# Kernel optimization log

Measured on AMD Instinct MI355X. Metric: run time of the kernel, lower is better.

## Reference

```python
import jax, jax.numpy as jnp
import numpy as np

B, N, D = 8, 2048, 1024

def setup_inputs() -> dict:
    key = jax.random.key(0)
    ks = jax.random.split(key, 7)
    s = 1.0 / np.sqrt(D)
    return {
        "x": jax.random.normal(ks[0], (B, N, D), dtype=jnp.float32),
        "Wq": jax.random.uniform(ks[1], (D, D), jnp.float32, -s, s),
        "bq": jax.random.uniform(ks[2], (D,), jnp.float32, -s, s),
        "Wk": jax.random.uniform(ks[3], (D, D), jnp.float32, -s, s),
        "bk": jax.random.uniform(ks[4], (D,), jnp.float32, -s, s),
        "Wv": jax.random.uniform(ks[5], (D, D), jnp.float32, -s, s),
        "bv": jax.random.uniform(ks[6], (D,), jnp.float32, -s, s),
    }

def reference(x, Wq, bq, Wk, bk, Wv, bv):
    # torch nn.Linear: y = x @ W.T + b
    q = jnp.einsum('bnd,ed->bne', x, Wq) + bq
    k = jnp.einsum('bnd,ed->bne', x, Wk) + bk
    v = jnp.einsum('bnd,ed->bne', x, Wv) + bv
    # NOTE: original applies NO 1/sqrt(d) scaling
    scores = jnp.einsum('bnd,bmd->bnm', q, k)  # [B, N, N]
    probs = jax.nn.softmax(scores, axis=-1)
    return jnp.einsum('bnm,bmd->bnd', probs, v)
```

## Files before the change

### kernel.cpp

```cpp
#include <hip/hip_runtime.h>


typedef _Float16 f16;
typedef _Float16 f16x4 __attribute__((ext_vector_type(4)));
typedef _Float16 f16x8 __attribute__((ext_vector_type(8)));
typedef float f32x4 __attribute__((ext_vector_type(4)));

#define Nn_ 2048
#define Dd 1024

typedef const __attribute__((address_space(1))) void gvoid;
typedef __attribute__((address_space(3))) void lvoid;

__device__ __forceinline__ void glds16(const void* g, void* l) {
    __builtin_amdgcn_global_load_lds((gvoid*)g, (lvoid*)l, 16, 0, 0);
}
__device__ __forceinline__ void bar_vm3() {
    asm volatile("s_waitcnt vmcnt(3)\n\ts_barrier" ::: "memory");
}
__device__ __forceinline__ void bar_vm0() {
    asm volatile("s_waitcnt vmcnt(0)\n\ts_barrier" ::: "memory");
}

__global__ void cvt_kernel(const float4* __restrict__ in, f16x4* __restrict__ out, int n4) {
    int i = blockIdx.x * 256 + threadIdx.x;
    if (i >= n4) return;
    float4 f = in[i];
    f16x4 h;
    h.x = (_Float16)f.x; h.y = (_Float16)f.y; h.z = (_Float16)f.z; h.w = (_Float16)f.w;
    out[i] = h;
}

__global__ void concat_bias(const float* __restrict__ bq, const float* __restrict__ bk,
                            const float* __restrict__ bv, float* __restrict__ o) {
    int i = blockIdx.x * 256 + threadIdx.x;
    if (i >= 3072) return;
    o[i] = (i < 1024) ? bq[i] : (i < 2048 ? bk[i - 1024] : bv[i - 2048]);
}

__global__ __launch_bounds__(512) void gemm_bt(
    const f16* __restrict__ A, const f16* __restrict__ Bm,
    const float* __restrict__ bias, void* __restrict__ Cout,
    f16* __restrict__ qh, f16* __restrict__ kh, f16* __restrict__ vT,
    int K, int lda, int ldb, int ldc, int mode,
    long aStride, long bStride, long cStride)
{
    __shared__ f16 sm[36864];
    const int tid = threadIdx.x;
    const int lane = tid & 63, wid = tid >> 6;
    const int quad = lane >> 4, l16 = lane & 15;
    const int wm = (wid & 1) * 64;
    const int wn = (wid >> 1) * 64;
    const long m0 = (long)blockIdx.x * 128, n0 = (long)blockIdx.y * 256;
    const int bz = blockIdx.z;
    A += (long)bz * aStride;
    Bm += (long)bz * bStride;

    const int la = tid, lb0 = tid, lb1 = tid + 512;
    const long arow = m0 + (la >> 2);
    const long brow0 = n0 + (lb0 >> 2), brow1 = n0 + (lb1 >> 2);
    const int colA  = ((la & 3) ^ ((la >> 3) & 3)) * 8;
    const int colB0 = ((lb0 & 3) ^ ((lb0 >> 3) & 3)) * 8;
    const int colB1 = ((lb1 & 3) ^ ((lb1 >> 3) & 3)) * 8;

    const f16* pa  = A + arow * lda + colA;
    const f16* pb0 = Bm + brow0 * ldb + colB0;
    const f16* pb1 = Bm + brow1 * ldb + colB1;

    const int fo = (quad ^ ((l16 >> 1) & 3)) * 8;

    f32x4 acc[4][4];
#pragma unroll
    for (int i = 0; i < 4; i++)
#pragma unroll
        for (int j = 0; j < 4; j++) acc[i][j] = 0.0f;

    const int nk = K >> 5;
    glds16(pa, sm + la * 8);
    glds16(pb0, sm + 4096 + lb0 * 8);
    glds16(pb1, sm + 4096 + lb1 * 8);
    if (nk > 1) {
        glds16(pa + 32, sm + 12288 + la * 8);
        glds16(pb0 + 32, sm + 16384 + lb0 * 8);
        glds16(pb1 + 32, sm + 16384 + lb1 * 8);
    }

    int cur = 0;
    for (int it = 0; it < nk; ++it) {
        if (it + 1 < nk) bar_vm3(); else bar_vm0();
        if (it + 2 < nk) {
            f16* dst = sm + ((cur >= 1) ? (cur - 1) : 2) * 12288;
            const int ko = (it + 2) * 32;
            glds16(pa + ko, dst + la * 8);
            glds16(pb0 + ko, dst + 4096 + lb0 * 8);
            glds16(pb1 + ko, dst + 4096 + lb1 * 8);
        }
        const f16* As = sm + cur * 12288;
        const f16* Bs = As + 4096;
        f16x8 af[4], bf[4];
#pragma unroll
        for (int rt = 0; rt < 4; rt++)
            af[rt] = *(const f16x8*)(As + (wm + rt * 16 + l16) * 32 + fo);
#pragma unroll
        for (int ct = 0; ct < 4; ct++)
            bf[ct] = *(const f16x8*)(Bs + (wn + ct * 16 + l16) * 32 + fo);
#pragma unroll
        for (int rt = 0; rt < 4; rt++)
#pragma unroll
            for (int ct = 0; ct < 4; ct++)
                acc[rt][ct] = __builtin_amdgcn_mfma_f32_16x16x32_f16(af[rt], bf[ct], acc[rt][ct], 0, 0, 0);
        cur = (cur == 2) ? 0 : cur + 1;
    }

    if (mode == 2) {
        float* O = (float*)Cout + (long)bz * cStride;
#pragma unroll
        for (int ct = 0; ct < 4; ct++) {
            long n = n0 + wn + ct * 16 + l16;
#pragma unroll
            for (int rt = 0; rt < 4; rt++) {
                long mb = m0 + wm + rt * 16 + quad * 4;
#pragma unroll
                for (int r = 0; r < 4; r++)
                    O[(mb + r) * ldc + n] = acc[rt][ct][r];
            }
        }
    } else {
        if (blockIdx.y < 8) {
            f16* O = (blockIdx.y < 4) ? qh : kh;
#pragma unroll
            for (int ct = 0; ct < 4; ct++) {
                long n = n0 + wn + ct * 16 + l16;
                float bs = bias[n];
                long n1 = n & 1023;
#pragma unroll
                for (int rt = 0; rt < 4; rt++) {
                    long mb = m0 + wm + rt * 16 + quad * 4;
#pragma unroll
                    for (int r = 0; r < 4; r++)
                        O[(mb + r) * 1024 + n1] = (f16)(acc[rt][ct][r] + bs);
                }
            }
        } else {
            const long nb = n0 - 2048;
            const long vbase = (m0 >> 11) * (long)(Dd * Nn_) + (m0 & 2047);
#pragma unroll
            for (int g = 0; g < 4; ++g) {
                __syncthreads();
                if ((wid >> 1) == g) {
#pragma unroll
                    for (int ct = 0; ct < 4; ++ct) {
                        int cl = ct * 16 + l16;
                        float bs = bias[n0 + g * 64 + cl];
#pragma unroll
                        for (int rt = 0; rt < 4; rt++) {
                            int row = wm + rt * 16 + quad * 4;
#pragma unroll
                            for (int r = 0; r < 4; r++)
                                sm[cl * 136 + row + r] = (f16)(acc[rt][ct][r] + bs);
                        }
                    }
                }
                __syncthreads();
                const int rowi = tid >> 3, c = (tid & 7) * 16;
                f16* dst = vT + vbase + (nb + g * 64 + rowi) * (long)Nn_ + c;
                const f16* src = sm + rowi * 136 + c;
                *(f16x8*)(dst) = *(const f16x8*)(src);
                *(f16x8*)(dst + 8) = *(const f16x8*)(src + 8);
            }
        }
    }
}

__global__ __launch_bounds__(256) void softmax_rows(float* __restrict__ S) {
    const int row = blockIdx.x * 4 + (threadIdx.x >> 6);
    const int lane = threadIdx.x & 63;
    float* Sr = S + (long)row * 2048;
    const float4* R4 = (const float4*)Sr;
    float4 t[8];
#pragma unroll
    for (int i = 0; i < 8; i++) t[i] = R4[lane + 64 * i];
    float mx = -1e30f;
#pragma unroll
    for (int i = 0; i < 8; i++)
        mx = fmaxf(mx, fmaxf(fmaxf(t[i].x, t[i].y), fmaxf(t[i].z, t[i].w)));
#pragma unroll
    for (int off = 1; off < 64; off <<= 1) mx = fmaxf(mx, __shfl_xor(mx, off, 64));
    float se = 0.0f;
#pragma unroll
    for (int i = 0; i < 8; i++) {
        t[i].x = __expf(t[i].x - mx); t[i].y = __expf(t[i].y - mx);
        t[i].z = __expf(t[i].z - mx); t[i].w = __expf(t[i].w - mx);
        se += t[i].x + t[i].y + t[i].z + t[i].w;
    }
#pragma unroll
    for (int off = 1; off < 64; off <<= 1) se += __shfl_xor(se, off, 64);
    const float li = 1.0f / se;
    f16x4* P4 = (f16x4*)Sr;
#pragma unroll
    for (int i = 0; i < 8; i++) {
        f16x4 h;
        h.x = (_Float16)(t[i].x * li); h.y = (_Float16)(t[i].y * li);
        h.z = (_Float16)(t[i].z * li); h.w = (_Float16)(t[i].w * li);
        P4[lane + 64 * i] = h;
    }
}

extern "C" void kernel_launch(void* const* d_in, const int* in_sizes, int n_in,
                              void* d_out, int out_size, void* d_ws, size_t ws_size,
                              hipStream_t stream) {
    const float* x  = (const float*)d_in[0];
    const float* Wq = (const float*)d_in[1];
    const float* bq = (const float*)d_in[2];
    const float* Wk = (const float*)d_in[3];
    const float* bk = (const float*)d_in[4];
    const float* Wv = (const float*)d_in[5];
    const float* bv = (const float*)d_in[6];

    f16* wsh = (f16*)d_ws;
    dim3 blk(512);
    const bool full = ws_size >= 234881024ULL;

    if (full) {
        f16* qh  = wsh;
        f16* kh  = wsh + 16777216;
        f16* vT  = wsh + 33554432;
        float* S = (float*)(wsh + 50331648);
        f16* xh  = wsh + 50331648;
        f16* Wh  = wsh + 67108864;
        float* bqkv = (float*)(wsh + 70254592);

        cvt_kernel<<<16384, 256, 0, stream>>>((const float4*)x, (f16x4*)xh, 4194304);
        cvt_kernel<<<1024, 256, 0, stream>>>((const float4*)Wq, (f16x4*)Wh, 262144);
        cvt_kernel<<<1024, 256, 0, stream>>>((const float4*)Wk, (f16x4*)(Wh + 1048576), 262144);
        cvt_kernel<<<1024, 256, 0, stream>>>((const float4*)Wv, (f16x4*)(Wh + 2097152), 262144);
        concat_bias<<<12, 256, 0, stream>>>(bq, bk, bv, bqkv);

        gemm_bt<<<dim3(128, 12, 1), blk, 0, stream>>>(
            xh, Wh, bqkv, nullptr, qh, kh, vT,
            1024, 1024, 1024, 0, 3, 0, 0, 0);
        gemm_bt<<<dim3(16, 8, 8), blk, 0, stream>>>(
            qh, kh, nullptr, S, nullptr, nullptr, nullptr,
            1024, 1024, 1024, 2048, 2,
            (long)Nn_ * Dd, (long)Nn_ * Dd, (long)Nn_ * Nn_);
        softmax_rows<<<4096, 256, 0, stream>>>(S);
        gemm_bt<<<dim3(16, 4, 8), blk, 0, stream>>>(
            (const f16*)S, vT, nullptr, d_out, nullptr, nullptr, nullptr,
            2048, 4096, 2048, 1024, 2,
            (long)Nn_ * 4096, (long)Dd * Nn_, (long)Nn_ * Dd);
    } else {
        f16* xh  = wsh;
        f16* Wh  = wsh + 16777216;
        float* bqkv = (float*)(wsh + 19922944);
        f16* qh  = wsh + 19929088;
        f16* kh  = qh + 16777216;
        f16* vT  = kh + 16777216;
        float* S = (float*)(vT + 16777216);

        cvt_kernel<<<16384, 256, 0, stream>>>((const float4*)x, (f16x4*)xh, 4194304);
        cvt_kernel<<<1024, 256, 0, stream>>>((const float4*)Wq, (f16x4*)Wh, 262144);
        cvt_kernel<<<1024, 256, 0, stream>>>((const float4*)Wk, (f16x4*)(Wh + 1048576), 262144);
        cvt_kernel<<<1024, 256, 0, stream>>>((const float4*)Wv, (f16x4*)(Wh + 2097152), 262144);
        concat_bias<<<12, 256, 0, stream>>>(bq, bk, bv, bqkv);

        gemm_bt<<<dim3(128, 12, 1), blk, 0, stream>>>(
            xh, Wh, bqkv, nullptr, qh, kh, vT,
            1024, 1024, 1024, 0, 3, 0, 0, 0);

        for (int h = 0; h < 2; ++h) {
            const long b0 = 4L * h;
            gemm_bt<<<dim3(16, 8, 4), blk, 0, stream>>>(
                qh + b0 * Nn_ * Dd, kh + b0 * Nn_ * Dd, nullptr, S,
                nullptr, nullptr, nullptr,
                1024, 1024, 1024, 2048, 2,
                (long)Nn_ * Dd, (long)Nn_ * Dd, (long)Nn_ * Nn_);
            softmax_rows<<<2048, 256, 0, stream>>>(S);
            gemm_bt<<<dim3(16, 4, 4), blk, 0, stream>>>(
                (const f16*)S, vT + b0 * Dd * Nn_, nullptr,
                (float*)d_out + b0 * Nn_ * Dd, nullptr, nullptr, nullptr,
                2048, 4096, 2048, 1024, 2,
                (long)Nn_ * 4096, (long)Dd * Nn_, (long)Nn_ * Dd);
        }
    }
}
```

Baseline: 449.7 us.

## Rewrite GEMM mainloop as 256x256x64 tile with interleaved loads and MFMA phases

The shared GEMM kernel moves from a 128x256 tile with K-step 32 and triple buffering to a 256x256 tile with K-step 64 and double buffering. Each K iteration is split into four MFMA quadrants, with global-to-LDS loads for later stages issued between them, s_setprio raised around the MFMA bursts, and an 8-way XOR swizzle. The aim is more arithmetic per byte loaded and better overlap of memory traffic with matrix work. In exchange it needs 128 KB of LDS, more accumulator registers and half as many blocks, which may reduce occupancy and leave CUs idle at the tail.

```diff
diff --git a/kernel.cpp b/kernel.cpp
--- a/kernel.cpp
+++ b/kernel.cpp
@@ -15,12 +15,13 @@
 __device__ __forceinline__ void glds16(const void* g, void* l) {
     __builtin_amdgcn_global_load_lds((gvoid*)g, (lvoid*)l, 16, 0, 0);
 }
-__device__ __forceinline__ void bar_vm3() {
-    asm volatile("s_waitcnt vmcnt(3)\n\ts_barrier" ::: "memory");
-}
-__device__ __forceinline__ void bar_vm0() {
-    asm volatile("s_waitcnt vmcnt(0)\n\ts_barrier" ::: "memory");
-}
+#define BARRIER()  asm volatile("s_barrier" ::: "memory")
+#define LGKM0()    asm volatile("s_waitcnt lgkmcnt(0)" ::: "memory")
+#define VM6()      asm volatile("s_waitcnt vmcnt(6)" ::: "memory")
+#define VM0()      asm volatile("s_waitcnt vmcnt(0)" ::: "memory")
+#define PRIO1()    __builtin_amdgcn_s_setprio(1)
+#define PRIO0()    __builtin_amdgcn_s_setprio(0)
+#define MFMA(a, b, c) __builtin_amdgcn_mfma_f32_16x16x32_f16((a), (b), (c), 0, 0, 0)
 
 __global__ void cvt_kernel(const float4* __restrict__ in, f16x4* __restrict__ out, int n4) {
     int i = blockIdx.x * 256 + threadIdx.x;
@@ -45,81 +46,145 @@
     int K, int lda, int ldb, int ldc, int mode,
     long aStride, long bStride, long cStride)
 {
-    __shared__ f16 sm[36864];
+    __shared__ f16 sm[65536];
     const int tid = threadIdx.x;
     const int lane = tid & 63, wid = tid >> 6;
     const int quad = lane >> 4, l16 = lane & 15;
-    const int wm = (wid & 1) * 64;
-    const int wn = (wid >> 1) * 64;
-    const long m0 = (long)blockIdx.x * 128, n0 = (long)blockIdx.y * 256;
-    const int bz = blockIdx.z;
-    A += (long)bz * aStride;
-    Bm += (long)bz * bStride;
-
-    const int la = tid, lb0 = tid, lb1 = tid + 512;
-    const long arow = m0 + (la >> 2);
-    const long brow0 = n0 + (lb0 >> 2), brow1 = n0 + (lb1 >> 2);
-    const int colA  = ((la & 3) ^ ((la >> 3) & 3)) * 8;
-    const int colB0 = ((lb0 & 3) ^ ((lb0 >> 3) & 3)) * 8;
-    const int colB1 = ((lb1 & 3) ^ ((lb1 >> 3) & 3)) * 8;
-
-    const f16* pa  = A + arow * lda + colA;
-    const f16* pb0 = Bm + brow0 * ldb + colB0;
-    const f16* pb1 = Bm + brow1 * ldb + colB1;
-
-    const int fo = (quad ^ ((l16 >> 1) & 3)) * 8;
-
-    f32x4 acc[4][4];
-#pragma unroll
-    for (int i = 0; i < 4; i++)
+    const int wm = wid & 1;
+    const int wn = wid >> 1;
+    const long m0 = (long)blockIdx.x * 256, n0 = (long)blockIdx.y * 256;
+    A += (long)blockIdx.z * aStride;
+    Bm += (long)blockIdx.z * bStride;
+
+    const int lr = tid >> 3;
+    const int sc8 = ((tid & 7) ^ (lr & 7)) * 8;
+    const f16* pa = A + (m0 + lr) * (long)lda + sc8;
+    const f16* pb = Bm + (n0 + lr) * (long)ldb + sc8;
+    const long a64 = 64L * lda, b64 = 64L * ldb;
+
+    const int aRow = (wm * 128 + l16) * 64;
+    const int bRow = (wn * 64 + l16) * 64;
+    const int co0 = (quad ^ (l16 & 7)) * 8;
+    const int co1 = ((quad + 4) ^ (l16 & 7)) * 8;
+
+    f32x4 acc[8][4];
+#pragma unroll
+    for (int i = 0; i < 8; i++)
 #pragma unroll
         for (int j = 0; j < 4; j++) acc[i][j] = 0.0f;
 
-    const int nk = K >> 5;
-    glds16(pa, sm + la * 8);
-    glds16(pb0, sm + 4096 + lb0 * 8);
-    glds16(pb1, sm + 4096 + lb1 * 8);
+    const int nk = K >> 6;
+
+#pragma unroll
+    for (int q = 0; q < 4; ++q) glds16(pa + q * a64, sm + tid * 8 + q * 4096);
+#pragma unroll
+    for (int q = 0; q < 4; ++q) glds16(pb + q * b64, sm + 16384 + tid * 8 + q * 4096);
     if (nk > 1) {
-        glds16(pa + 32, sm + 12288 + la * 8);
-        glds16(pb0 + 32, sm + 16384 + lb0 * 8);
-        glds16(pb1 + 32, sm + 16384 + lb1 * 8);
-    }
-
-    int cur = 0;
-    for (int it = 0; it < nk; ++it) {
-        if (it + 1 < nk) bar_vm3(); else bar_vm0();
-        if (it + 2 < nk) {
-            f16* dst = sm + ((cur >= 1) ? (cur - 1) : 2) * 12288;
-            const int ko = (it + 2) * 32;
-            glds16(pa + ko, dst + la * 8);
-            glds16(pb0 + ko, dst + 4096 + lb0 * 8);
-            glds16(pb1 + ko, dst + 4096 + lb1 * 8);
-        }
-        const f16* As = sm + cur * 12288;
-        const f16* Bs = As + 4096;
-        f16x8 af[4], bf[4];
-#pragma unroll
-        for (int rt = 0; rt < 4; rt++)
-            af[rt] = *(const f16x8*)(As + (wm + rt * 16 + l16) * 32 + fo);
-#pragma unroll
-        for (int ct = 0; ct < 4; ct++)
-            bf[ct] = *(const f16x8*)(Bs + (wn + ct * 16 + l16) * 32 + fo);
-#pragma unroll
-        for (int rt = 0; rt < 4; rt++)
-#pragma unroll
-            for (int ct = 0; ct < 4; ct++)
-                acc[rt][ct] = __builtin_amdgcn_mfma_f32_16x16x32_f16(af[rt], bf[ct], acc[rt][ct], 0, 0, 0);
-        cur = (cur == 2) ? 0 : cur + 1;
+        glds16(pa + 0 * a64 + 64, sm + 32768 + tid * 8);
+        glds16(pa + 2 * a64 + 64, sm + 32768 + tid * 8 + 2 * 4096);
+#pragma unroll
+        for (int q = 0; q < 4; ++q)
+            glds16(pb + q * b64 + 64, sm + 32768 + 16384 + tid * 8 + q * 4096);
+        VM6(); BARRIER();
+    } else {
+        VM0(); BARRIER();
+    }
+
+    f16x8 af[2][4], bf0[2][2], bf1[2][2];
+    for (int t = 0; t < nk; ++t) {
+        const int bo = (t & 1) << 15;
+        const int bn = bo ^ 32768;
+        const f16* As = sm + bo;
+        const f16* Bs = As + 16384;
+        const long kt1 = (long)(t + 1) * 64, kt2 = (long)(t + 2) * 64;
+
+#pragma unroll
+        for (int i = 0; i < 4; ++i) {
+            af[0][i] = *(const f16x8*)(As + aRow + i * 1024 + co0);
+            af[1][i] = *(const f16x8*)(As + aRow + i * 1024 + co1);
+        }
+#pragma unroll
+        for (int j = 0; j < 2; ++j) {
+            bf0[0][j] = *(const f16x8*)(Bs + bRow + j * 1024 + co0);
+            bf0[1][j] = *(const f16x8*)(Bs + bRow + j * 1024 + co1);
+        }
+        if (t + 1 < nk) {
+            glds16(pa + 1 * a64 + kt1, sm + bn + tid * 8 + 1 * 4096);
+            glds16(pa + 3 * a64 + kt1, sm + bn + tid * 8 + 3 * 4096);
+        }
+        BARRIER(); LGKM0(); PRIO1();
+#pragma unroll
+        for (int i = 0; i < 4; ++i)
+#pragma unroll
+            for (int j = 0; j < 2; ++j) {
+                acc[i][j] = MFMA(af[0][i], bf0[0][j], acc[i][j]);
+                acc[i][j] = MFMA(af[1][i], bf0[1][j], acc[i][j]);
+            }
+        PRIO0(); BARRIER();
+
+#pragma unroll
+        for (int j = 0; j < 2; ++j) {
+            bf1[0][j] = *(const f16x8*)(Bs + bRow + 2048 + j * 1024 + co0);
+            bf1[1][j] = *(const f16x8*)(Bs + bRow + 2048 + j * 1024 + co1);
+        }
+        if (t + 2 < nk) {
+            glds16(pa + 0 * a64 + kt2, sm + bo + tid * 8);
+            glds16(pa + 2 * a64 + kt2, sm + bo + tid * 8 + 2 * 4096);
+        }
+        BARRIER(); LGKM0(); PRIO1();
+#pragma unroll
+        for (int i = 0; i < 4; ++i)
+#pragma unroll
+            for (int j = 0; j < 2; ++j) {
+                acc[i][2 + j] = MFMA(af[0][i], bf1[0][j], acc[i][2 + j]);
+                acc[i][2 + j] = MFMA(af[1][i], bf1[1][j], acc[i][2 + j]);
+            }
+        PRIO0(); BARRIER();
+
+#pragma unroll
+        for (int i = 0; i < 4; ++i) {
+            af[0][i] = *(const f16x8*)(As + aRow + 4096 + i * 1024 + co0);
+            af[1][i] = *(const f16x8*)(As + aRow + 4096 + i * 1024 + co1);
+        }
+        if (t + 2 < nk) {
+            glds16(pb + 0 * b64 + kt2, sm + bo + 16384 + tid * 8);
+            glds16(pb + 1 * b64 + kt2, sm + bo + 16384 + tid * 8 + 4096);
+        }
+        BARRIER(); LGKM0(); PRIO1();
+#pragma unroll
+        for (int i = 0; i < 4; ++i)
+#pragma unroll
+            for (int j = 0; j < 2; ++j) {
+                acc[4 + i][j] = MFMA(af[0][i], bf0[0][j], acc[4 + i][j]);
+                acc[4 + i][j] = MFMA(af[1][i], bf0[1][j], acc[4 + i][j]);
+            }
+        PRIO0(); BARRIER();
+
+        if (t + 2 < nk) {
+            glds16(pb + 2 * b64 + kt2, sm + bo + 16384 + tid * 8 + 2 * 4096);
+            glds16(pb + 3 * b64 + kt2, sm + bo + 16384 + tid * 8 + 3 * 4096);
+        }
+        BARRIER(); PRIO1();
+#pragma unroll
+        for (int i = 0; i < 4; ++i)
+#pragma unroll
+            for (int j = 0; j < 2; ++j) {
+                acc[4 + i][2 + j] = MFMA(af[0][i], bf1[0][j], acc[4 + i][2 + j]);
+                acc[4 + i][2 + j] = MFMA(af[1][i], bf1[1][j], acc[4 + i][2 + j]);
+            }
+        PRIO0();
+        if (t + 2 < nk) { VM6(); } else { VM0(); }
+        BARRIER();
     }
 
     if (mode == 2) {
-        float* O = (float*)Cout + (long)bz * cStride;
+        float* O = (float*)Cout + (long)blockIdx.z * cStride;
 #pragma unroll
         for (int ct = 0; ct < 4; ct++) {
-            long n = n0 + wn + ct * 16 + l16;
-#pragma unroll
-            for (int rt = 0; rt < 4; rt++) {
-                long mb = m0 + wm + rt * 16 + quad * 4;
+            long n = n0 + wn * 64 + ct * 16 + l16;
+#pragma unroll
+            for (int rt = 0; rt < 8; rt++) {
+                long mb = m0 + wm * 128 + rt * 16 + quad * 4;
 #pragma unroll
                 for (int r = 0; r < 4; r++)
                     O[(mb + r) * ldc + n] = acc[rt][ct][r];
@@ -130,12 +195,12 @@
             f16* O = (blockIdx.y < 4) ? qh : kh;
 #pragma unroll
             for (int ct = 0; ct < 4; ct++) {
-                long n = n0 + wn + ct * 16 + l16;
+                long n = n0 + wn * 64 + ct * 16 + l16;
                 float bs = bias[n];
                 long n1 = n & 1023;
 #pragma unroll
-                for (int rt = 0; rt < 4; rt++) {
-                    long mb = m0 + wm + rt * 16 + quad * 4;
+                for (int rt = 0; rt < 8; rt++) {
+                    long mb = m0 + wm * 128 + rt * 16 + quad * 4;
 #pragma unroll
                     for (int r = 0; r < 4; r++)
                         O[(mb + r) * 1024 + n1] = (f16)(acc[rt][ct][r] + bs);
@@ -147,26 +212,28 @@
 #pragma unroll
             for (int g = 0; g < 4; ++g) {
                 __syncthreads();
-                if ((wid >> 1) == g) {
+                if (wn == g) {
 #pragma unroll
                     for (int ct = 0; ct < 4; ++ct) {
                         int cl = ct * 16 + l16;
                         float bs = bias[n0 + g * 64 + cl];
 #pragma unroll
-                        for (int rt = 0; rt < 4; rt++) {
-                            int row = wm + rt * 16 + quad * 4;
+                        for (int rt = 0; rt < 8; rt++) {
+                            int row = wm * 128 + rt * 16 + quad * 4;
 #pragma unroll
                             for (int r = 0; r < 4; r++)
-                                sm[cl * 136 + row + r] = (f16)(acc[rt][ct][r] + bs);
+                                sm[cl * 264 + row + r] = (f16)(acc[rt][ct][r] + bs);
                         }
                     }
                 }
                 __syncthreads();
-                const int rowi = tid >> 3, c = (tid & 7) * 16;
+                const int rowi = tid >> 3, c = (tid & 7) * 32;
                 f16* dst = vT + vbase + (nb + g * 64 + rowi) * (long)Nn_ + c;
-                const f16* src = sm + rowi * 136 + c;
+                const f16* src = sm + rowi * 264 + c;
                 *(f16x8*)(dst) = *(const f16x8*)(src);
                 *(f16x8*)(dst + 8) = *(const f16x8*)(src + 8);
+                *(f16x8*)(dst + 16) = *(const f16x8*)(src + 16);
+                *(f16x8*)(dst + 24) = *(const f16x8*)(src + 24);
             }
         }
     }
@@ -236,15 +303,15 @@
         cvt_kernel<<<1024, 256, 0, stream>>>((const float4*)Wv, (f16x4*)(Wh + 2097152), 262144);
         concat_bias<<<12, 256, 0, stream>>>(bq, bk, bv, bqkv);
 
-        gemm_bt<<<dim3(128, 12, 1), blk, 0, stream>>>(
+        gemm_bt<<<dim3(64, 12, 1), blk, 0, stream>>>(
             xh, Wh, bqkv, nullptr, qh, kh, vT,
             1024, 1024, 1024, 0, 3, 0, 0, 0);
-        gemm_bt<<<dim3(16, 8, 8), blk, 0, stream>>>(
+        gemm_bt<<<dim3(8, 8, 8), blk, 0, stream>>>(
             qh, kh, nullptr, S, nullptr, nullptr, nullptr,
             1024, 1024, 1024, 2048, 2,
             (long)Nn_ * Dd, (long)Nn_ * Dd, (long)Nn_ * Nn_);
         softmax_rows<<<4096, 256, 0, stream>>>(S);
-        gemm_bt<<<dim3(16, 4, 8), blk, 0, stream>>>(
+        gemm_bt<<<dim3(8, 4, 8), blk, 0, stream>>>(
             (const f16*)S, vT, nullptr, d_out, nullptr, nullptr, nullptr,
             2048, 4096, 2048, 1024, 2,
             (long)Nn_ * 4096, (long)Dd * Nn_, (long)Nn_ * Dd);
@@ -263,19 +330,19 @@
         cvt_kernel<<<1024, 256, 0, stream>>>((const float4*)Wv, (f16x4*)(Wh + 2097152), 262144);
         concat_bias<<<12, 256, 0, stream>>>(bq, bk, bv, bqkv);
 
-        gemm_bt<<<dim3(128, 12, 1), blk, 0, stream>>>(
+        gemm_bt<<<dim3(64, 12, 1), blk, 0, stream>>>(
             xh, Wh, bqkv, nullptr, qh, kh, vT,
             1024, 1024, 1024, 0, 3, 0, 0, 0);
 
         for (int h = 0; h < 2; ++h) {
             const long b0 = 4L * h;
-            gemm_bt<<<dim3(16, 8, 4), blk, 0, stream>>>(
+            gemm_bt<<<dim3(8, 8, 4), blk, 0, stream>>>(
                 qh + b0 * Nn_ * Dd, kh + b0 * Nn_ * Dd, nullptr, S,
                 nullptr, nullptr, nullptr,
                 1024, 1024, 1024, 2048, 2,
                 (long)Nn_ * Dd, (long)Nn_ * Dd, (long)Nn_ * Nn_);
             softmax_rows<<<2048, 256, 0, stream>>>(S);
-            gemm_bt<<<dim3(16, 4, 4), blk, 0, stream>>>(
+            gemm_bt<<<dim3(8, 4, 4), blk, 0, stream>>>(
                 (const f16*)S, vT + b0 * Dd * Nn_, nullptr,
                 (float*)d_out + b0 * Nn_ * Dd, nullptr, nullptr, nullptr,
                 2048, 4096, 2048, 1024, 2,
```

Result: faster. 434.2 us (-3.4%).
